# Kernel optimization log

Hardware: AMD Instinct MI355X
Metric: run time of the kernel (lower is better)

## Reference

```python
import jax, jax.numpy as jnp
import numpy as np

D_MODEL = 1024
N_HEADS = 16
D_HEAD = D_MODEL // N_HEADS


def setup_inputs() -> dict:
    key = jax.random.key(0)
    ks = jax.random.split(key, 5)
    scale = 1.0 / np.sqrt(D_MODEL)
    return {
        "x": jax.random.normal(ks[0], (2, 2048, D_MODEL), dtype=jnp.float32),
        "W_q": jax.random.normal(ks[1], (D_MODEL, D_MODEL), dtype=jnp.float32) * scale,
        "W_k": jax.random.normal(ks[2], (D_MODEL, D_MODEL), dtype=jnp.float32) * scale,
        "W_v": jax.random.normal(ks[3], (D_MODEL, D_MODEL), dtype=jnp.float32) * scale,
        "W_o": jax.random.normal(ks[4], (D_MODEL, D_MODEL), dtype=jnp.float32) * scale,
    }


def reference(x, W_q, W_k, W_v, W_o):
    B, S, _ = x.shape
    # nn.Linear computes x @ W.T; weights stored [out, in]
    def proj(W):
        y = jnp.einsum("bsd,ed->bse", x, W)
        return y.reshape(B, S, N_HEADS, D_HEAD).transpose(0, 2, 1, 3)  # [B,H,S,Dh]

    q, k, v = proj(W_q), proj(W_k), proj(W_v)
    scores = jnp.einsum("bhqd,bhkd->bhqk", q, k) / jnp.sqrt(jnp.float32(D_HEAD))
    causal = jnp.triu(jnp.ones((S, S), dtype=bool), k=1)
    scores = jnp.where(causal, -jnp.inf, scores)
    attn = jax.nn.softmax(scores, axis=-1)
    out = jnp.einsum("bhqk,bhkd->bhqd", attn, v)  # [B,H,S,Dh]
    out = out.transpose(0, 2, 1, 3).reshape(B, S, D_MODEL)
    return jnp.einsum("bsd,ed->bse", out, W_o)
```

## Files before the change

kernel.cpp:

```cpp
#include <hip/hip_runtime.h>


#define DMODEL 1024
#define NHEADS 16
#define DHEAD  64
#define SEQ    2048
#define BATCH  2
#define MROWS  (BATCH * SEQ)

typedef __bf16 bf16x8 __attribute__((ext_vector_type(8)));
typedef __bf16 bf16x4 __attribute__((ext_vector_type(4)));
typedef float  f32x4  __attribute__((ext_vector_type(4)));

__device__ __forceinline__ f32x4 mfma16(bf16x8 a, bf16x8 b, f32x4 c) {
    return __builtin_amdgcn_mfma_f32_16x16x32_bf16(a, b, c, 0, 0, 0);
}

__device__ __forceinline__ bf16x8 ld8(const float* p) {
    const f32x4 a0 = *(const f32x4*)p;
    const f32x4 a1 = *(const f32x4*)(p + 4);
    bf16x8 v;
    v[0] = (__bf16)a0[0]; v[1] = (__bf16)a0[1];
    v[2] = (__bf16)a0[2]; v[3] = (__bf16)a0[3];
    v[4] = (__bf16)a1[0]; v[5] = (__bf16)a1[1];
    v[6] = (__bf16)a1[2]; v[7] = (__bf16)a1[3];
    return v;
}

__device__ __forceinline__ void gll16(const __bf16* g, __bf16* l) {
    __builtin_amdgcn_global_load_lds(
        (const __attribute__((address_space(1))) void*)g,
        (__attribute__((address_space(3))) void*)l,
        16, 0, 0);
}

__global__ __launch_bounds__(256) void cvt_kernel(const float* __restrict__ x,
                                                  const float* __restrict__ Wq,
                                                  const float* __restrict__ Wk,
                                                  const float* __restrict__ Wv,
                                                  const float* __restrict__ Wo,
                                                  __bf16* __restrict__ xb,
                                                  __bf16* __restrict__ wcat) {
    const int c = blockIdx.x * 256 + threadIdx.x;
    if (c < 524288) {
        *(bf16x8*)(xb + (size_t)c * 8) = ld8(x + (size_t)c * 8);
    } else {
        const int i = c - 524288;
        const int w = i >> 17;
        const int j = i & 131071;
        const float* src = (w == 0) ? Wq : (w == 1) ? Wk : (w == 2) ? Wv : Wo;
        *(bf16x8*)(wcat + (size_t)w * DMODEL * DMODEL + (size_t)j * 8) =
            ld8(src + (size_t)j * 8);
    }
}

template <typename TC, int MREP, int NREP>
__device__ __forceinline__ void gemm_bb_body(const __bf16* __restrict__ A,
                                             const __bf16* __restrict__ W,
                                             TC* __restrict__ C,
                                             __bf16* __restrict__ VT,
                                             bool vt, int m0, int bn0, int cn0,
                                             float scale) {
    constexpr int K  = DMODEL;
    constexpr int TM = MREP * 32;
    constexpr int TN = NREP * 32;
    __shared__ __align__(16) __bf16 As[2][TM][32];
    __shared__ __align__(16) __bf16 Bs[2][TN][32];

    const int tid  = threadIdx.x;
    const int lane = tid & 63;
    const int wave = tid >> 6;
    const int quad = lane >> 4;
    const int l16  = lane & 15;
    const int wm   = wave & 1;
    const int wn   = wave >> 1;

    const int srow = lane >> 2;
    const int scol = (lane & 3) * 8;

    const __bf16* ap = A + (size_t)(m0 + srow) * K + scol;
    const __bf16* bp = W + (size_t)(bn0 + srow) * K + scol;

    f32x4 acc[MREP][NREP] = {};

#pragma unroll
    for (int j = 0; j < MREP / 2; ++j) {
        const int r = wave * (MREP * 8) + j * 16;
        gll16(ap + (size_t)r * K, &As[0][r][0]);
    }
#pragma unroll
    for (int j = 0; j < NREP / 2; ++j) {
        const int r = wave * (NREP * 8) + j * 16;
        gll16(bp + (size_t)r * K, &Bs[0][r][0]);
    }
    __syncthreads();

    int cur = 0;
    for (int k0 = 0; k0 < K; k0 += 32) {
        if (k0 + 32 < K) {
            const int kn = k0 + 32;
#pragma unroll
            for (int j = 0; j < MREP / 2; ++j) {
                const int r = wave * (MREP * 8) + j * 16;
                gll16(ap + (size_t)r * K + kn, &As[cur ^ 1][r][0]);
            }
#pragma unroll
            for (int j = 0; j < NREP / 2; ++j) {
                const int r = wave * (NREP * 8) + j * 16;
                gll16(bp + (size_t)r * K + kn, &Bs[cur ^ 1][r][0]);
            }
        }

        bf16x8 af[MREP], bfr[NREP];
#pragma unroll
        for (int i = 0; i < MREP; ++i)
            af[i] = *(const bf16x8*)(&As[cur][wm * (MREP * 16) + i * 16 + l16][quad * 8]);
#pragma unroll
        for (int j = 0; j < NREP; ++j)
            bfr[j] = *(const bf16x8*)(&Bs[cur][wn * (NREP * 16) + j * 16 + l16][quad * 8]);
#pragma unroll
        for (int mi = 0; mi < MREP; ++mi)
#pragma unroll
            for (int ni = 0; ni < NREP; ++ni)
                acc[mi][ni] = mfma16(af[mi], bfr[ni], acc[mi][ni]);

        __syncthreads();
        cur ^= 1;
    }

    if (!vt) {
#pragma unroll
        for (int mi = 0; mi < MREP; ++mi)
#pragma unroll
            for (int ni = 0; ni < NREP; ++ni)
#pragma unroll
                for (int r = 0; r < 4; ++r) {
                    int row = m0 + wm * (MREP * 16) + mi * 16 + quad * 4 + r;
                    int col = cn0 + wn * (NREP * 16) + ni * 16 + l16;
                    C[(size_t)row * DMODEL + col] = (TC)(acc[mi][ni][r] * scale);
                }
    } else {
#pragma unroll
        for (int mi = 0; mi < MREP; ++mi)
#pragma unroll
            for (int ni = 0; ni < NREP; ++ni) {
                const int m  = m0 + wm * (MREP * 16) + mi * 16 + quad * 4;
                const int hd = cn0 + wn * (NREP * 16) + ni * 16 + l16;
                bf16x4 v4;
#pragma unroll
                for (int r = 0; r < 4; ++r) v4[r] = (__bf16)acc[mi][ni][r];
                *(bf16x4*)(VT + (size_t)hd * MROWS + m) = v4;
            }
    }
}

#define QSCALE 0.1803368801111204f

__global__ __launch_bounds__(256) void qkv_kernel(const __bf16* __restrict__ X,
                                                  const __bf16* __restrict__ wcat,
                                                  __bf16* __restrict__ Q,
                                                  __bf16* __restrict__ K,
                                                  __bf16* __restrict__ VT) {
    const int bn0 = blockIdx.x * 256;
    const int z   = bn0 >> 10;
    const int cn0 = bn0 - (z << 10);
    __bf16* Y = (z == 0) ? Q : K;
    const float scale = (z == 0) ? QSCALE : 1.0f;
    gemm_bb_body<__bf16, 4, 8>(X, wcat, Y, VT, z == 2,
                               blockIdx.y * 128, bn0, cn0, scale);
}

__global__ __launch_bounds__(256) void out_gemm_kernel(const __bf16* __restrict__ A,
                                                       const __bf16* __restrict__ W,
                                                       float* __restrict__ C) {
    gemm_bb_body<float, 2, 4>(A, W, C, nullptr, false,
                              blockIdx.y * 64, blockIdx.x * 128, blockIdx.x * 128,
                              1.0f);
}

__global__ __launch_bounds__(256) void attn_kernel(const __bf16* __restrict__ Q,
                                                   const __bf16* __restrict__ Kg,
                                                   const __bf16* __restrict__ VTg,
                                                   __bf16* __restrict__ O) {
    const int bh  = blockIdx.x;
    const int y   = blockIdx.y;
    const int ya  = y >> 3, yr = y & 7;
    const int qt2 = (ya == 0) ? (31 - yr)
                  : (ya == 1) ? (16 + yr)
                  : (ya == 2) ? (15 - yr)
                  :             yr;
    const int b = bh >> 4, h = bh & 15;
    const size_t base = (size_t)b * SEQ * DMODEL + (size_t)h * DHEAD;

    const int tid  = threadIdx.x;
    const int lane = tid & 63;
    const int wave = tid >> 6;
    const int quad = lane >> 4;
    const int l16  = lane & 15;

    __shared__ __align__(16) __bf16 Ks[64][64];
    __shared__ __align__(16) __bf16 Vs[64][64];
    __shared__ __align__(16) __bf16 Ps[4][2][16][40];

    const int sr = lane >> 3;
    const int sc = ((lane & 7) ^ sr) * 8;

    const int qrow = qt2 * 64 + wave * 16 + l16;

    const bf16x8 qf0 = *(const bf16x8*)(Q + base + (size_t)qrow * DMODEL + quad * 8);
    const bf16x8 qf1 = *(const bf16x8*)(Q + base + (size_t)qrow * DMODEL + 32 + quad * 8);

    const __bf16* kp = Kg + base + (size_t)(wave * 16 + sr) * DMODEL + sc;
    const __bf16* vp = VTg + (size_t)(h * 64 + wave * 16 + sr) * MROWS
                           + (size_t)b * SEQ + sc;

    bf16x8 ones;
#pragma unroll
    for (int i = 0; i < 8; ++i) ones[i] = (__bf16)1.0f;

    f32x4 oacc[4] = {};
    f32x4 lacc = {};

    const int ntiles = qt2 + 1;
    const int gsw = (l16 & 7);

    for (int kt = 0; kt < ntiles; ++kt) {
        const int k0 = kt * 64;
        __syncthreads();
        {
            const __bf16* kpt = kp + (size_t)k0 * DMODEL;
            const __bf16* vpt = vp + k0;
            gll16(kpt, &Ks[wave * 16][0]);
            gll16(kpt + (size_t)8 * DMODEL, &Ks[wave * 16 + 8][0]);
            gll16(vpt, &Vs[wave * 16][0]);
            gll16(vpt + (size_t)8 * MROWS, &Vs[wave * 16 + 8][0]);
        }
        __syncthreads();

        const bool diag = (kt == ntiles - 1);

        f32x4 s[4];
#pragma unroll
        for (int g = 0; g < 4; ++g) {
            const bf16x8 kfa = *(const bf16x8*)(&Ks[g * 16 + l16][(quad ^ gsw) * 8]);
            const bf16x8 kfb = *(const bf16x8*)(&Ks[g * 16 + l16][((quad + 4) ^ gsw) * 8]);
            f32x4 t = {};
            t = mfma16(kfa, qf0, t);
            t = mfma16(kfb, qf1, t);
            s[g] = t;
        }

        bf16x4 w4[4];
        if (!diag) {
#pragma unroll
            for (int g = 0; g < 4; ++g)
#pragma unroll
                for (int r = 0; r < 4; ++r)
                    w4[g][r] = (__bf16)exp2f(s[g][r]);
        } else {
#pragma unroll
            for (int g = 0; g < 4; ++g)
#pragma unroll
                for (int r = 0; r < 4; ++r) {
                    const int kk = k0 + g * 16 + quad * 4 + r;
                    w4[g][r] = (kk <= qrow) ? (__bf16)exp2f(s[g][r]) : (__bf16)0.f;
                }
        }

#pragma unroll
        for (int g = 0; g < 4; ++g)
            *(bf16x4*)(&Ps[wave][g >> 1][l16][(g & 1) * 16 + quad * 4]) = w4[g];

        const bf16x8 pf0 = *(const bf16x8*)(&Ps[wave][0][l16][quad * 8]);
        const bf16x8 pf1 = *(const bf16x8*)(&Ps[wave][1][l16][quad * 8]);
        lacc = mfma16(ones, pf0, lacc);
        lacc = mfma16(ones, pf1, lacc);
#pragma unroll
        for (int f = 0; f < 4; ++f) {
            const bf16x8 vfa = *(const bf16x8*)(&Vs[f * 16 + l16][(quad ^ gsw) * 8]);
            const bf16x8 vfb = *(const bf16x8*)(&Vs[f * 16 + l16][((quad + 4) ^ gsw) * 8]);
            f32x4 t = oacc[f];
            t = mfma16(vfa, pf0, t);
            t = mfma16(vfb, pf1, t);
            oacc[f] = t;
        }
    }

    const float l_i = lacc[0];
    const float inv = (l_i > 0.f) ? (1.f / l_i) : 0.f;
#pragma unroll
    for (int f = 0; f < 4; ++f) {
        bf16x4 o;
#pragma unroll
        for (int r = 0; r < 4; ++r) o[r] = (__bf16)(oacc[f][r] * inv);
        *(bf16x4*)(O + base + (size_t)qrow * DMODEL + f * 16 + quad * 4) = o;
    }
}

extern "C" void kernel_launch(void* const* d_in, const int* in_sizes, int n_in,
                              void* d_out, int out_size, void* d_ws, size_t ws_size,
                              hipStream_t stream) {
    const float* x  = (const float*)d_in[0];
    const float* Wq = (const float*)d_in[1];
    const float* Wk = (const float*)d_in[2];
    const float* Wv = (const float*)d_in[3];
    const float* Wo = (const float*)d_in[4];
    float* out = (float*)d_out;

    const size_t tm = (size_t)MROWS * DMODEL;
    const size_t tw = (size_t)DMODEL * DMODEL;
    __bf16* Q    = (__bf16*)d_ws;
    __bf16* K    = Q + tm;
    __bf16* VT   = K + tm;
    __bf16* xb   = VT + tm;
    __bf16* wcat = xb + tm;

    cvt_kernel<<<4096, 256, 0, stream>>>(x, Wq, Wk, Wv, Wo, xb, wcat);

    dim3 g1(3072 / 256, MROWS / 128);
    qkv_kernel<<<g1, 256, 0, stream>>>(xb, wcat, Q, K, VT);

    dim3 g2(BATCH * NHEADS, SEQ / 64);
    attn_kernel<<<g2, 256, 0, stream>>>(Q, K, VT, Q);

    dim3 g3(DMODEL / 128, MROWS / 64);
    out_gemm_kernel<<<g3, 256, 0, stream>>>(Q, wcat + 3 * tw, out);
}
```

Baseline: 214.0 us.

## Double-buffer K/V tiles in attention and shrink QKV GEMM tile width

```diff
diff --git a/kernel.cpp b/kernel.cpp
--- a/kernel.cpp
+++ b/kernel.cpp
@@ -161,12 +161,12 @@
                                                   __bf16* __restrict__ Q,
                                                   __bf16* __restrict__ K,
                                                   __bf16* __restrict__ VT) {
-    const int bn0 = blockIdx.x * 256;
+    const int bn0 = blockIdx.x * 128;
     const int z   = bn0 >> 10;
     const int cn0 = bn0 - (z << 10);
     __bf16* Y = (z == 0) ? Q : K;
     const float scale = (z == 0) ? QSCALE : 1.0f;
-    gemm_bb_body<__bf16, 4, 8>(X, wcat, Y, VT, z == 2,
+    gemm_bb_body<__bf16, 4, 4>(X, wcat, Y, VT, z == 2,
                                blockIdx.y * 128, bn0, cn0, scale);
 }
 
@@ -198,8 +198,8 @@
     const int quad = lane >> 4;
     const int l16  = lane & 15;
 
-    __shared__ __align__(16) __bf16 Ks[64][64];
-    __shared__ __align__(16) __bf16 Vs[64][64];
+    __shared__ __align__(16) __bf16 Ks[2][64][64];
+    __shared__ __align__(16) __bf16 Vs[2][64][64];
     __shared__ __align__(16) __bf16 Ps[4][2][16][40];
 
     const int sr = lane >> 3;
@@ -224,26 +224,32 @@
     const int ntiles = qt2 + 1;
     const int gsw = (l16 & 7);
 
+    gll16(kp, &Ks[0][wave * 16][0]);
+    gll16(kp + (size_t)8 * DMODEL, &Ks[0][wave * 16 + 8][0]);
+    gll16(vp, &Vs[0][wave * 16][0]);
+    gll16(vp + (size_t)8 * MROWS, &Vs[0][wave * 16 + 8][0]);
+    __syncthreads();
+
+    int cur = 0;
     for (int kt = 0; kt < ntiles; ++kt) {
         const int k0 = kt * 64;
-        __syncthreads();
-        {
-            const __bf16* kpt = kp + (size_t)k0 * DMODEL;
-            const __bf16* vpt = vp + k0;
-            gll16(kpt, &Ks[wave * 16][0]);
-            gll16(kpt + (size_t)8 * DMODEL, &Ks[wave * 16 + 8][0]);
-            gll16(vpt, &Vs[wave * 16][0]);
-            gll16(vpt + (size_t)8 * MROWS, &Vs[wave * 16 + 8][0]);
-        }
-        __syncthreads();
+
+        if (kt + 1 < ntiles) {
+            const __bf16* kpt = kp + (size_t)(k0 + 64) * DMODEL;
+            const __bf16* vpt = vp + (k0 + 64);
+            gll16(kpt, &Ks[cur ^ 1][wave * 16][0]);
+            gll16(kpt + (size_t)8 * DMODEL, &Ks[cur ^ 1][wave * 16 + 8][0]);
+            gll16(vpt, &Vs[cur ^ 1][wave * 16][0]);
+            gll16(vpt + (size_t)8 * MROWS, &Vs[cur ^ 1][wave * 16 + 8][0]);
+        }
 
         const bool diag = (kt == ntiles - 1);
 
         f32x4 s[4];
 #pragma unroll
         for (int g = 0; g < 4; ++g) {
-            const bf16x8 kfa = *(const bf16x8*)(&Ks[g * 16 + l16][(quad ^ gsw) * 8]);
-            const bf16x8 kfb = *(const bf16x8*)(&Ks[g * 16 + l16][((quad + 4) ^ gsw) * 8]);
+            const bf16x8 kfa = *(const bf16x8*)(&Ks[cur][g * 16 + l16][(quad ^ gsw) * 8]);
+            const bf16x8 kfb = *(const bf16x8*)(&Ks[cur][g * 16 + l16][((quad + 4) ^ gsw) * 8]);
             f32x4 t = {};
             t = mfma16(kfa, qf0, t);
             t = mfma16(kfb, qf1, t);
@@ -277,13 +283,16 @@
         lacc = mfma16(ones, pf1, lacc);
 #pragma unroll
         for (int f = 0; f < 4; ++f) {
-            const bf16x8 vfa = *(const bf16x8*)(&Vs[f * 16 + l16][(quad ^ gsw) * 8]);
-            const bf16x8 vfb = *(const bf16x8*)(&Vs[f * 16 + l16][((quad + 4) ^ gsw) * 8]);
+            const bf16x8 vfa = *(const bf16x8*)(&Vs[cur][f * 16 + l16][(quad ^ gsw) * 8]);
+            const bf16x8 vfb = *(const bf16x8*)(&Vs[cur][f * 16 + l16][((quad + 4) ^ gsw) * 8]);
             f32x4 t = oacc[f];
             t = mfma16(vfa, pf0, t);
             t = mfma16(vfb, pf1, t);
             oacc[f] = t;
         }
+
+        __syncthreads();
+        cur ^= 1;
     }
 
     const float l_i = lacc[0];
@@ -317,7 +326,7 @@
 
     cvt_kernel<<<4096, 256, 0, stream>>>(x, Wq, Wk, Wv, Wo, xb, wcat);
 
-    dim3 g1(3072 / 256, MROWS / 128);
+    dim3 g1(3072 / 128, MROWS / 128);
     qkv_kernel<<<g1, 256, 0, stream>>>(xb, wcat, Q, K, VT);
 
     dim3 g2(BATCH * NHEADS, SEQ / 64);
```

Measured after the change: 183.2 us. 14.4% less time.
